# Kernel optimization log

Hardware: AMD Instinct MI355X
Metric: run time of the kernel (lower is better)

Reference implementation:

```python
import jax, jax.numpy as jnp
import numpy as np


def setup_inputs() -> dict:
    key = jax.random.key(0)
    ks = jax.random.split(key, 6)
    B, H, N, C, O, G = 4, 24, 512, 120, 512, 5
    x = jax.random.normal(ks[0], (B, H, N, C), dtype=jnp.float32)
    t_indices = jnp.arange(H, dtype=jnp.int64)
    time_emb = jax.random.normal(ks[1], (H, 8), dtype=jnp.float32)
    # kaiming-uniform-ish init for base linear weight
    fan_in = C + 8
    bound = float(np.sqrt(6.0 / fan_in))
    base_w = jax.random.uniform(ks[2], (O, C + 8), minval=-bound, maxval=bound, dtype=jnp.float32)
    base_b = jax.random.uniform(ks[3], (O,), minval=-1.0 / np.sqrt(fan_in), maxval=1.0 / np.sqrt(fan_in), dtype=jnp.float32)
    spline_weight = jax.random.uniform(ks[4], (O, C + 8, G), minval=-0.1, maxval=0.1, dtype=jnp.float32)
    return {"x": x, "t_indices": t_indices, "time_emb": time_emb,
            "base_w": base_w, "base_b": base_b, "spline_weight": spline_weight}


def reference(x, t_indices, time_emb, base_w, base_b, spline_weight):
    B, H, N, C = x.shape
    G = spline_weight.shape[-1]
    grid = jnp.linspace(-1.0, 1.0, G, dtype=x.dtype)  # non-trainable buffer
    # time embedding lookup, broadcast over batch and nodes: [B,H,N,8]
    t_emb = jnp.broadcast_to(time_emb[t_indices][None, :, None, :], (B, H, N, time_emb.shape[-1]))
    x_in = jnp.concatenate([x, t_emb], axis=-1)  # [B,H,N,C+8]
    # base path: SiLU then linear
    base = jnp.einsum('bhni,oi->bhno', jax.nn.silu(x_in), base_w) + base_b
    # RBF basis: [B,H,N,C+8,G]
    inv_h = (G - 1) / 2.0  # 1 / (2/(G-1))
    basis = jnp.exp(-(((x_in[..., None] - grid) * inv_h) ** 2))
    spline = jnp.einsum('bhnig,oig->bhno', basis, spline_weight)
    return base + spline
```

## Files before the change

### kernel.cpp

```cpp
#include <hip/hip_runtime.h>
#include <hip/hip_bf16.h>

typedef __attribute__((ext_vector_type(4))) float f32x4;
typedef __attribute__((ext_vector_type(8))) short bf16x8;

#define GLDS16(gp, lp) __builtin_amdgcn_global_load_lds( \
    (__attribute__((address_space(1))) void*)(void*)(gp), \
    (__attribute__((address_space(3))) void*)(lp), 16, 0, 0)

static constexpr int Mtot = 4 * 24 * 512;
static constexpr int Ktot = 128 * 6;
static constexpr int Otot = 512;
static constexpr int Hh   = 24;
static constexpr int Cc   = 120;

__device__ inline unsigned short f2bf(float f) {
    __hip_bfloat16 h = __float2bfloat16(f);
    unsigned short u;
    __builtin_memcpy(&u, &h, 2);
    return u;
}

__global__ __launch_bounds__(256) void prep_A(
        const float* __restrict__ x, const int* __restrict__ t_idx,
        const float* __restrict__ temb, unsigned int* __restrict__ A)
{
    int tid = blockIdx.x * 256 + threadIdx.x;
    int i = tid & 127;
    int m = tid >> 7;
    int h = (m >> 9) % Hh;
    float v;
    if (i < Cc) v = x[m * Cc + i];
    else        v = temb[t_idx[h] * 8 + (i - Cc)];
    float f[6];
    f[0] = v / (1.0f + __expf(-v));
    #pragma unroll
    for (int g = 0; g < 5; ++g) {
        float t2 = 2.0f * (v - (-1.0f + 0.5f * g));
        f[1 + g] = __expf(-t2 * t2);
    }
    A[tid * 3 + 0] = f2bf(f[0]) | ((unsigned)f2bf(f[1]) << 16);
    A[tid * 3 + 1] = f2bf(f[2]) | ((unsigned)f2bf(f[3]) << 16);
    A[tid * 3 + 2] = f2bf(f[4]) | ((unsigned)f2bf(f[5]) << 16);
}

__global__ __launch_bounds__(256) void prep_W(
        const float* __restrict__ bw, const float* __restrict__ sw,
        unsigned int* __restrict__ Wt)
{
    int tid = blockIdx.x * 256 + threadIdx.x;
    float f[6];
    f[0] = bw[tid];
    #pragma unroll
    for (int g = 0; g < 5; ++g) f[1 + g] = sw[tid * 5 + g];
    Wt[tid * 3 + 0] = f2bf(f[0]) | ((unsigned)f2bf(f[1]) << 16);
    Wt[tid * 3 + 1] = f2bf(f[2]) | ((unsigned)f2bf(f[3]) << 16);
    Wt[tid * 3 + 2] = f2bf(f[4]) | ((unsigned)f2bf(f[5]) << 16);
}

__global__ __launch_bounds__(256) void gemm_kan(
        const __hip_bfloat16* __restrict__ A,
        const __hip_bfloat16* __restrict__ W,
        const float* __restrict__ bias,
        float* __restrict__ out)
{
    __shared__ __hip_bfloat16 As[128 * 32];
    __shared__ __hip_bfloat16 Bs[128 * 32];
    const int t    = threadIdx.x;
    const int wave = t >> 6;
    const int lane = t & 63;
    const int m_base = blockIdx.x * 128;
    const int n_base = blockIdx.y * 128;
    const int wm = (wave >> 1) * 64;
    const int wn = (wave & 1) * 64;

    f32x4 acc[4][4] = {};

    const __hip_bfloat16* ag0 = A + (long)(m_base +      (t >> 2)) * Ktot + (t & 3) * 8;
    const __hip_bfloat16* ag1 = A + (long)(m_base + 64 + (t >> 2)) * Ktot + (t & 3) * 8;
    const __hip_bfloat16* bg0 = W + (long)(n_base +      (t >> 2)) * Ktot + (t & 3) * 8;
    const __hip_bfloat16* bg1 = W + (long)(n_base + 64 + (t >> 2)) * Ktot + (t & 3) * 8;

    char* AsB = (char*)As;
    char* BsB = (char*)Bs;
    char* lA0 = AsB +        wave * 1024;
    char* lA1 = AsB + 4096 + wave * 1024;
    char* lB0 = BsB +        wave * 1024;
    char* lB1 = BsB + 4096 + wave * 1024;

    const char* pa = AsB + (wm + (lane & 15)) * 64 + (lane >> 4) * 16;
    const char* pb = BsB + (wn + (lane & 15)) * 64 + (lane >> 4) * 16;

    for (int kt = 0; kt < Ktot; kt += 32) {
        GLDS16(ag0 + kt, lA0);
        GLDS16(ag1 + kt, lA1);
        GLDS16(bg0 + kt, lB0);
        GLDS16(bg1 + kt, lB1);
        __syncthreads();
        bf16x8 af[4], bf[4];
        #pragma unroll
        for (int mi = 0; mi < 4; ++mi) af[mi] = *(const bf16x8*)(pa + mi * 16 * 64);
        #pragma unroll
        for (int ni = 0; ni < 4; ++ni) bf[ni] = *(const bf16x8*)(pb + ni * 16 * 64);
        #pragma unroll
        for (int mi = 0; mi < 4; ++mi)
            #pragma unroll
            for (int ni = 0; ni < 4; ++ni)
                acc[mi][ni] = __builtin_amdgcn_mfma_f32_16x16x32_bf16(
                    af[mi], bf[ni], acc[mi][ni], 0, 0, 0);
        __syncthreads();
    }

    const int col0 = n_base + wn + (lane & 15);
    const int row0 = m_base + wm + (lane >> 4) * 4;
    #pragma unroll
    for (int ni = 0; ni < 4; ++ni) {
        const int col = col0 + ni * 16;
        const float bv = bias[col];
        #pragma unroll
        for (int mi = 0; mi < 4; ++mi) {
            #pragma unroll
            for (int r = 0; r < 4; ++r) {
                out[(long)(row0 + mi * 16 + r) * Otot + col] = acc[mi][ni][r] + bv;
            }
        }
    }
}

extern "C" void kernel_launch(void* const* d_in, const int* in_sizes, int n_in,
                              void* d_out, int out_size, void* d_ws, size_t ws_size,
                              hipStream_t stream) {
    const float* x    = (const float*)d_in[0];
    const int*   tidx = (const int*)  d_in[1];
    const float* temb = (const float*)d_in[2];
    const float* bw   = (const float*)d_in[3];
    const float* bb   = (const float*)d_in[4];
    const float* sw   = (const float*)d_in[5];
    float* out = (float*)d_out;

    __hip_bfloat16* A  = (__hip_bfloat16*)d_ws;
    __hip_bfloat16* Wt = (__hip_bfloat16*)((char*)d_ws + (size_t)Mtot * Ktot * 2);

    prep_A<<<Mtot * 128 / 256, 256, 0, stream>>>(x, tidx, temb, (unsigned int*)A);
    prep_W<<<Otot * 128 / 256, 256, 0, stream>>>(bw, sw, (unsigned int*)Wt);
    gemm_kan<<<dim3(Mtot / 128, Otot / 128), 256, 0, stream>>>(A, Wt, bb, out);
}
```

Before: 197.4 us.

## Widen GEMM tile to 128x256 with K=64 swizzled LDS and vectorize prep_A

The GEMM now uses a 128x256 output tile per block, with each wave computing 64x128. Each iteration stages a K step of 64 into XOR-swizzled LDS, which raises operand reuse, halves the barrier count and avoids bank conflicts. prep_A now has each thread process four features with one float4 load and uint4 stores, cutting per-thread overhead and narrow memory transactions. The trade-offs are more accumulator registers, with launch bounds asking for 2 blocks per SM, and fewer GEMM blocks: 768 instead of 1536, which could hurt load balance.

Result: no change. 197.7 us (+0.2%).

```diff
diff --git a/kernel.cpp b/kernel.cpp
--- a/kernel.cpp
+++ b/kernel.cpp
@@ -12,7 +12,6 @@
 static constexpr int Ktot = 128 * 6;
 static constexpr int Otot = 512;
 static constexpr int Hh   = 24;
-static constexpr int Cc   = 120;
 
 __device__ inline unsigned short f2bf(float f) {
     __hip_bfloat16 h = __float2bfloat16(f);
@@ -21,27 +20,39 @@
     return u;
 }
 
-__global__ __launch_bounds__(256) void prep_A(
-        const float* __restrict__ x, const int* __restrict__ t_idx,
-        const float* __restrict__ temb, unsigned int* __restrict__ A)
-{
-    int tid = blockIdx.x * 256 + threadIdx.x;
-    int i = tid & 127;
-    int m = tid >> 7;
-    int h = (m >> 9) % Hh;
-    float v;
-    if (i < Cc) v = x[m * Cc + i];
-    else        v = temb[t_idx[h] * 8 + (i - Cc)];
-    float f[6];
-    f[0] = v / (1.0f + __expf(-v));
+__device__ inline void feat6(float v, unsigned* o) {
+    float f0 = v / (1.0f + __expf(-v));
+    float r[5];
     #pragma unroll
     for (int g = 0; g < 5; ++g) {
         float t2 = 2.0f * (v - (-1.0f + 0.5f * g));
-        f[1 + g] = __expf(-t2 * t2);
+        r[g] = __expf(-t2 * t2);
     }
-    A[tid * 3 + 0] = f2bf(f[0]) | ((unsigned)f2bf(f[1]) << 16);
-    A[tid * 3 + 1] = f2bf(f[2]) | ((unsigned)f2bf(f[3]) << 16);
-    A[tid * 3 + 2] = f2bf(f[4]) | ((unsigned)f2bf(f[5]) << 16);
+    o[0] = f2bf(f0)   | ((unsigned)f2bf(r[0]) << 16);
+    o[1] = f2bf(r[1]) | ((unsigned)f2bf(r[2]) << 16);
+    o[2] = f2bf(r[3]) | ((unsigned)f2bf(r[4]) << 16);
+}
+
+__global__ __launch_bounds__(256) void prep_A(
+        const float* __restrict__ x, const int* __restrict__ t_idx,
+        const float* __restrict__ temb, uint4* __restrict__ A4)
+{
+    int tid = blockIdx.x * 256 + threadIdx.x;
+    int j = tid & 31;
+    int m = tid >> 5;
+    int h = (m >> 9) % Hh;
+    float4 v4;
+    if (j < 30) v4 = *(const float4*)(x + m * 120 + j * 4);
+    else        v4 = *(const float4*)(temb + t_idx[h] * 8 + (j - 30) * 4);
+    unsigned o[12];
+    feat6(v4.x, o + 0);
+    feat6(v4.y, o + 3);
+    feat6(v4.z, o + 6);
+    feat6(v4.w, o + 9);
+    uint4* dst = A4 + tid * 3;
+    dst[0] = make_uint4(o[0], o[1], o[2], o[3]);
+    dst[1] = make_uint4(o[4], o[5], o[6], o[7]);
+    dst[2] = make_uint4(o[8], o[9], o[10], o[11]);
 }
 
 __global__ __launch_bounds__(256) void prep_W(
@@ -58,63 +69,69 @@
     Wt[tid * 3 + 2] = f2bf(f[4]) | ((unsigned)f2bf(f[5]) << 16);
 }
 
-__global__ __launch_bounds__(256) void gemm_kan(
+__global__ __launch_bounds__(256, 2) void gemm_kan(
         const __hip_bfloat16* __restrict__ A,
         const __hip_bfloat16* __restrict__ W,
         const float* __restrict__ bias,
         float* __restrict__ out)
 {
-    __shared__ __hip_bfloat16 As[128 * 32];
-    __shared__ __hip_bfloat16 Bs[128 * 32];
+    __shared__ char AsB[128 * 128];
+    __shared__ char BsB[256 * 128];
     const int t    = threadIdx.x;
     const int wave = t >> 6;
     const int lane = t & 63;
     const int m_base = blockIdx.x * 128;
-    const int n_base = blockIdx.y * 128;
+    const int n_base = blockIdx.y * 256;
     const int wm = (wave >> 1) * 64;
-    const int wn = (wave & 1) * 64;
+    const int wn = (wave & 1) * 128;
+    const int ll = lane & 15;
+    const int q4 = lane >> 4;
 
-    f32x4 acc[4][4] = {};
+    f32x4 acc[4][8] = {};
 
-    const __hip_bfloat16* ag0 = A + (long)(m_base +      (t >> 2)) * Ktot + (t & 3) * 8;
-    const __hip_bfloat16* ag1 = A + (long)(m_base + 64 + (t >> 2)) * Ktot + (t & 3) * 8;
-    const __hip_bfloat16* bg0 = W + (long)(n_base +      (t >> 2)) * Ktot + (t & 3) * 8;
-    const __hip_bfloat16* bg1 = W + (long)(n_base + 64 + (t >> 2)) * Ktot + (t & 3) * 8;
+    const int lr = t >> 3;
+    const int s8 = t & 7;
+    const int cg = s8 ^ (lr & 7);
+    const __hip_bfloat16* ag = A + (long)(m_base + lr) * Ktot + cg * 8;
+    const __hip_bfloat16* bg = W + (long)(n_base + lr) * Ktot + cg * 8;
+    char* ldsA = AsB + wave * 1024;
+    char* ldsB = BsB + wave * 1024;
 
-    char* AsB = (char*)As;
-    char* BsB = (char*)Bs;
-    char* lA0 = AsB +        wave * 1024;
-    char* lA1 = AsB + 4096 + wave * 1024;
-    char* lB0 = BsB +        wave * 1024;
-    char* lB1 = BsB + 4096 + wave * 1024;
+    const int coff = ((q4 ^ (ll & 7)) * 16);
+    const int aoff = (wm + ll) * 128 + coff;
+    const int boff = (wn + ll) * 128 + coff;
 
-    const char* pa = AsB + (wm + (lane & 15)) * 64 + (lane >> 4) * 16;
-    const char* pb = BsB + (wn + (lane & 15)) * 64 + (lane >> 4) * 16;
-
-    for (int kt = 0; kt < Ktot; kt += 32) {
-        GLDS16(ag0 + kt, lA0);
-        GLDS16(ag1 + kt, lA1);
-        GLDS16(bg0 + kt, lB0);
-        GLDS16(bg1 + kt, lB1);
+    for (int kt = 0; kt < Ktot; kt += 64) {
+        #pragma unroll
+        for (int q = 0; q < 4; ++q)
+            GLDS16(ag + kt + (long)q * 32 * Ktot, ldsA + q * 4096);
+        #pragma unroll
+        for (int q = 0; q < 8; ++q)
+            GLDS16(bg + kt + (long)q * 32 * Ktot, ldsB + q * 4096);
         __syncthreads();
-        bf16x8 af[4], bf[4];
         #pragma unroll
-        for (int mi = 0; mi < 4; ++mi) af[mi] = *(const bf16x8*)(pa + mi * 16 * 64);
-        #pragma unroll
-        for (int ni = 0; ni < 4; ++ni) bf[ni] = *(const bf16x8*)(pb + ni * 16 * 64);
-        #pragma unroll
-        for (int mi = 0; mi < 4; ++mi)
+        for (int kk = 0; kk < 2; ++kk) {
+            const int ao = kk ? (aoff ^ 64) : aoff;
+            const int bo = kk ? (boff ^ 64) : boff;
+            bf16x8 af[4], bf[8];
             #pragma unroll
-            for (int ni = 0; ni < 4; ++ni)
-                acc[mi][ni] = __builtin_amdgcn_mfma_f32_16x16x32_bf16(
-                    af[mi], bf[ni], acc[mi][ni], 0, 0, 0);
+            for (int mi = 0; mi < 4; ++mi) af[mi] = *(const bf16x8*)(AsB + ao + mi * 2048);
+            #pragma unroll
+            for (int ni = 0; ni < 8; ++ni) bf[ni] = *(const bf16x8*)(BsB + bo + ni * 2048);
+            #pragma unroll
+            for (int mi = 0; mi < 4; ++mi)
+                #pragma unroll
+                for (int ni = 0; ni < 8; ++ni)
+                    acc[mi][ni] = __builtin_amdgcn_mfma_f32_16x16x32_bf16(
+                        af[mi], bf[ni], acc[mi][ni], 0, 0, 0);
+        }
         __syncthreads();
     }
 
-    const int col0 = n_base + wn + (lane & 15);
-    const int row0 = m_base + wm + (lane >> 4) * 4;
+    const int col0 = n_base + wn + ll;
+    const int row0 = m_base + wm + q4 * 4;
     #pragma unroll
-    for (int ni = 0; ni < 4; ++ni) {
+    for (int ni = 0; ni < 8; ++ni) {
         const int col = col0 + ni * 16;
         const float bv = bias[col];
         #pragma unroll
@@ -141,7 +158,7 @@
     __hip_bfloat16* A  = (__hip_bfloat16*)d_ws;
     __hip_bfloat16* Wt = (__hip_bfloat16*)((char*)d_ws + (size_t)Mtot * Ktot * 2);
 
-    prep_A<<<Mtot * 128 / 256, 256, 0, stream>>>(x, tidx, temb, (unsigned int*)A);
+    prep_A<<<Mtot * 32 / 256, 256, 0, stream>>>(x, tidx, temb, (uint4*)A);
     prep_W<<<Otot * 128 / 256, 256, 0, stream>>>(bw, sw, (unsigned int*)Wt);
-    gemm_kan<<<dim3(Mtot / 128, Otot / 128), 256, 0, stream>>>(A, Wt, bb, out);
+    gemm_kan<<<dim3(Mtot / 128, Otot / 256), 256, 0, stream>>>(A, Wt, bb, out);
 }
```

## Fuse SiLU/RBF basis expansion into GEMM A-tile producer, drop prep_A

Applied to the files above, without the earlier changes.

Removes the separate prep_A kernel that materialized the bf16 basis-expanded activation matrix in global memory. The GEMM now computes SiLU and the five RBF features on the fly from x/time_emb and writes them into an XOR-swizzled LDS tile with a larger K step (96 per iteration). Weights are pre-packed into a matching swizzled layout. The goal is to avoid the large intermediate write and read, at the cost of recomputing the features for each of the four N-column blocks and using more LDS per block.

Result: faster. 173.6 us (-12.0%).

```diff
diff --git a/kernel.cpp b/kernel.cpp
--- a/kernel.cpp
+++ b/kernel.cpp
@@ -8,11 +8,9 @@
     (__attribute__((address_space(1))) void*)(void*)(gp), \
     (__attribute__((address_space(3))) void*)(lp), 16, 0, 0)
 
-static constexpr int Mtot = 4 * 24 * 512;
-static constexpr int Ktot = 128 * 6;
+static constexpr int Mtot = 49152;
 static constexpr int Otot = 512;
 static constexpr int Hh   = 24;
-static constexpr int Cc   = 120;
 
 __device__ inline unsigned short f2bf(float f) {
     __hip_bfloat16 h = __float2bfloat16(f);
@@ -21,51 +19,40 @@
     return u;
 }
 
-__global__ __launch_bounds__(256) void prep_A(
-        const float* __restrict__ x, const int* __restrict__ t_idx,
-        const float* __restrict__ temb, unsigned int* __restrict__ A)
+__global__ __launch_bounds__(256) void prep_W(
+        const float* __restrict__ bw, const float* __restrict__ sw,
+        uint4* __restrict__ Wt)
 {
     int tid = blockIdx.x * 256 + threadIdx.x;
-    int i = tid & 127;
-    int m = tid >> 7;
-    int h = (m >> 9) % Hh;
-    float v;
-    if (i < Cc) v = x[m * Cc + i];
-    else        v = temb[t_idx[h] * 8 + (i - Cc)];
-    float f[6];
-    f[0] = v / (1.0f + __expf(-v));
-    #pragma unroll
-    for (int g = 0; g < 5; ++g) {
-        float t2 = 2.0f * (v - (-1.0f + 0.5f * g));
-        f[1 + g] = __expf(-t2 * t2);
+    int p    = tid & 15;
+    int o    = (tid >> 4) & 511;
+    int iter = tid >> 13;
+    int ck = p ^ (o & 7);
+    unsigned u[4] = {0u, 0u, 0u, 0u};
+    if (ck < 12) {
+        unsigned short s[8];
+        #pragma unroll
+        for (int e = 0; e < 8; ++e) {
+            int k = iter * 96 + ck * 8 + e;
+            int i = k / 6, f = k - i * 6;
+            float v = (f == 0) ? bw[o * 128 + i] : sw[(o * 128 + i) * 5 + (f - 1)];
+            s[e] = f2bf(v);
+        }
+        #pragma unroll
+        for (int n = 0; n < 4; ++n) u[n] = s[2 * n] | ((unsigned)s[2 * n + 1] << 16);
     }
-    A[tid * 3 + 0] = f2bf(f[0]) | ((unsigned)f2bf(f[1]) << 16);
-    A[tid * 3 + 1] = f2bf(f[2]) | ((unsigned)f2bf(f[3]) << 16);
-    A[tid * 3 + 2] = f2bf(f[4]) | ((unsigned)f2bf(f[5]) << 16);
+    Wt[tid] = make_uint4(u[0], u[1], u[2], u[3]);
 }
 
-__global__ __launch_bounds__(256) void prep_W(
-        const float* __restrict__ bw, const float* __restrict__ sw,
-        unsigned int* __restrict__ Wt)
-{
-    int tid = blockIdx.x * 256 + threadIdx.x;
-    float f[6];
-    f[0] = bw[tid];
-    #pragma unroll
-    for (int g = 0; g < 5; ++g) f[1 + g] = sw[tid * 5 + g];
-    Wt[tid * 3 + 0] = f2bf(f[0]) | ((unsigned)f2bf(f[1]) << 16);
-    Wt[tid * 3 + 1] = f2bf(f[2]) | ((unsigned)f2bf(f[3]) << 16);
-    Wt[tid * 3 + 2] = f2bf(f[4]) | ((unsigned)f2bf(f[5]) << 16);
-}
-
-__global__ __launch_bounds__(256) void gemm_kan(
-        const __hip_bfloat16* __restrict__ A,
-        const __hip_bfloat16* __restrict__ W,
+__global__ __launch_bounds__(256, 2) void gemm_kan(
+        const float* __restrict__ x, const int* __restrict__ t_idx,
+        const float* __restrict__ temb,
+        const char* __restrict__ Wt,
         const float* __restrict__ bias,
         float* __restrict__ out)
 {
-    __shared__ __hip_bfloat16 As[128 * 32];
-    __shared__ __hip_bfloat16 Bs[128 * 32];
+    __shared__ char AsB[128 * 256];
+    __shared__ char BsB[128 * 256];
     const int t    = threadIdx.x;
     const int wave = t >> 6;
     const int lane = t & 63;
@@ -73,46 +60,92 @@
     const int n_base = blockIdx.y * 128;
     const int wm = (wave >> 1) * 64;
     const int wn = (wave & 1) * 64;
+    const int ll = lane & 15;
+    const int q4 = lane >> 4;
 
     f32x4 acc[4][4] = {};
 
-    const __hip_bfloat16* ag0 = A + (long)(m_base +      (t >> 2)) * Ktot + (t & 3) * 8;
-    const __hip_bfloat16* ag1 = A + (long)(m_base + 64 + (t >> 2)) * Ktot + (t & 3) * 8;
-    const __hip_bfloat16* bg0 = W + (long)(n_base +      (t >> 2)) * Ktot + (t & 3) * 8;
-    const __hip_bfloat16* bg1 = W + (long)(n_base + 64 + (t >> 2)) * Ktot + (t & 3) * 8;
+    const char* bsrc0 = Wt + (size_t)n_base * 256 + t * 16;
+    char* ldsB = BsB + wave * 1024;
 
-    char* AsB = (char*)As;
-    char* BsB = (char*)Bs;
-    char* lA0 = AsB +        wave * 1024;
-    char* lA1 = AsB + 4096 + wave * 1024;
-    char* lB0 = BsB +        wave * 1024;
-    char* lB1 = BsB + 4096 + wave * 1024;
+    const int row = t >> 1;
+    const int oct = t & 1;
+    const int ht  = t_idx[(m_base >> 9) % Hh];
+    const float* xrow = x + (size_t)(m_base + row) * 120;
+    const float* trow = temb + ht * 8;
 
-    const char* pa = AsB + (wm + (lane & 15)) * 64 + (lane >> 4) * 16;
-    const char* pb = BsB + (wn + (lane & 15)) * 64 + (lane >> 4) * 16;
+    float4 xa, xb;
+    {
+        const int i0 = 8 * oct;
+        xa = *(const float4*)(xrow + i0);
+        xb = *(const float4*)(xrow + i0 + 4);
+    }
 
-    for (int kt = 0; kt < Ktot; kt += 32) {
-        GLDS16(ag0 + kt, lA0);
-        GLDS16(ag1 + kt, lA1);
-        GLDS16(bg0 + kt, lB0);
-        GLDS16(bg1 + kt, lB1);
+    for (int it = 0; it < 8; ++it) {
+        const char* bsrc = bsrc0 + (size_t)it * (512 * 256);
+        #pragma unroll
+        for (int q = 0; q < 8; ++q)
+            GLDS16(bsrc + q * 4096, ldsB + q * 4096);
+
+        float v[8];
+        v[0] = xa.x; v[1] = xa.y; v[2] = xa.z; v[3] = xa.w;
+        v[4] = xb.x; v[5] = xb.y; v[6] = xb.z; v[7] = xb.w;
+
+        if (it < 7) {
+            const int i0 = (it + 1) * 16 + 8 * oct;
+            const float* p = (i0 < 120) ? (xrow + i0) : (trow + (i0 - 120));
+            xa = *(const float4*)p;
+            xb = *(const float4*)(p + 4);
+        }
+
+        unsigned short s[48];
+        #pragma unroll
+        for (int c = 0; c < 8; ++c) {
+            const float vv = v[c];
+            s[c * 6 + 0] = f2bf(vv * __builtin_amdgcn_rcpf(1.0f + __expf(-vv)));
+            #pragma unroll
+            for (int g = 0; g < 5; ++g) {
+                const float d = 2.0f * (vv - (-1.0f + 0.5f * g));
+                s[c * 6 + 1 + g] = f2bf(__expf(-d * d));
+            }
+        }
+        #pragma unroll
+        for (int j = 0; j < 6; ++j) {
+            const int ck = 6 * oct + j;
+            const int phys = ck ^ (row & 7);
+            unsigned u[4];
+            #pragma unroll
+            for (int n = 0; n < 4; ++n)
+                u[n] = s[j * 8 + 2 * n] | ((unsigned)s[j * 8 + 2 * n + 1] << 16);
+            *(uint4*)(AsB + row * 256 + phys * 16) = make_uint4(u[0], u[1], u[2], u[3]);
+        }
         __syncthreads();
-        bf16x8 af[4], bf[4];
+
         #pragma unroll
-        for (int mi = 0; mi < 4; ++mi) af[mi] = *(const bf16x8*)(pa + mi * 16 * 64);
-        #pragma unroll
-        for (int ni = 0; ni < 4; ++ni) bf[ni] = *(const bf16x8*)(pb + ni * 16 * 64);
-        #pragma unroll
-        for (int mi = 0; mi < 4; ++mi)
+        for (int kk = 0; kk < 3; ++kk) {
+            bf16x8 af[4], bf[4];
             #pragma unroll
-            for (int ni = 0; ni < 4; ++ni)
-                acc[mi][ni] = __builtin_amdgcn_mfma_f32_16x16x32_bf16(
-                    af[mi], bf[ni], acc[mi][ni], 0, 0, 0);
+            for (int mi = 0; mi < 4; ++mi) {
+                const int r = wm + mi * 16 + ll;
+                af[mi] = *(const bf16x8*)(AsB + r * 256 + (((kk * 4 + q4) ^ (ll & 7)) * 16));
+            }
+            #pragma unroll
+            for (int ni = 0; ni < 4; ++ni) {
+                const int r = wn + ni * 16 + ll;
+                bf[ni] = *(const bf16x8*)(BsB + r * 256 + (((kk * 4 + q4) ^ (ll & 7)) * 16));
+            }
+            #pragma unroll
+            for (int mi = 0; mi < 4; ++mi)
+                #pragma unroll
+                for (int ni = 0; ni < 4; ++ni)
+                    acc[mi][ni] = __builtin_amdgcn_mfma_f32_16x16x32_bf16(
+                        af[mi], bf[ni], acc[mi][ni], 0, 0, 0);
+        }
         __syncthreads();
     }
 
-    const int col0 = n_base + wn + (lane & 15);
-    const int row0 = m_base + wm + (lane >> 4) * 4;
+    const int col0 = n_base + wn + ll;
+    const int row0 = m_base + wm + q4 * 4;
     #pragma unroll
     for (int ni = 0; ni < 4; ++ni) {
         const int col = col0 + ni * 16;
@@ -138,10 +171,9 @@
     const float* sw   = (const float*)d_in[5];
     float* out = (float*)d_out;
 
-    __hip_bfloat16* A  = (__hip_bfloat16*)d_ws;
-    __hip_bfloat16* Wt = (__hip_bfloat16*)((char*)d_ws + (size_t)Mtot * Ktot * 2);
+    char* Wt = (char*)d_ws;
 
-    prep_A<<<Mtot * 128 / 256, 256, 0, stream>>>(x, tidx, temb, (unsigned int*)A);
-    prep_W<<<Otot * 128 / 256, 256, 0, stream>>>(bw, sw, (unsigned int*)Wt);
-    gemm_kan<<<dim3(Mtot / 128, Otot / 128), 256, 0, stream>>>(A, Wt, bb, out);
+    prep_W<<<65536 / 256, 256, 0, stream>>>(bw, sw, (uint4*)Wt);
+    gemm_kan<<<dim3(Mtot / 128, Otot / 128), 256, 0, stream>>>(
+        x, tidx, temb, Wt, bb, out);
 }
```
